# Kernel tuning notes

Hardware: AMD Instinct MI355X
Metric: run time of the kernel (lower is better)

## Reference

```python
import jax, jax.numpy as jnp
import numpy as np

RATIO = 1.0 / 32  # spacial_ratio
HOUT = 7          # pooled_h
WOUT = 7          # pooled_w
S = 2             # sub_bin_size = int(sqrt(n_sampled=4))


def setup_inputs() -> dict:
    key = jax.random.key(0)
    k1, k2, k3, k4, k5, k6 = jax.random.split(key, 6)
    B, C, H, W = 4, 256, 50, 50
    N = 1024
    img_w, img_h = W / RATIO, H / RATIO
    features = jax.random.normal(k1, (B, C, H, W), dtype=jnp.float32)
    b = jax.random.randint(k2, (N,), 0, B).astype(jnp.float32)
    x1 = jax.random.uniform(k3, (N,), minval=0.0, maxval=img_w - 232.0)
    y1 = jax.random.uniform(k4, (N,), minval=0.0, maxval=img_h - 232.0)
    bw = jax.random.uniform(k5, (N,), minval=32.0, maxval=232.0)
    bh = jax.random.uniform(k6, (N,), minval=32.0, maxval=232.0)
    rois = jnp.stack([b, x1, y1, x1 + bw, y1 + bh], axis=1)  # [N, 5]
    return {"features": features, "rois": rois}


def _roi_align(features, rois):
    B, C, H, W = features.shape
    fW = jnp.float32(W)
    fH = jnp.float32(H)
    b_idx = rois[:, 0].astype(jnp.int32)            # [N]
    box = rois[:, 1:] * RATIO                       # [N, 4] in feature coords
    bx1 = jnp.clip(box[:, 0], 0.0, fW)
    by1 = jnp.clip(box[:, 1], 0.0, fH)
    bx2 = jnp.clip(box[:, 2], 0.0, fW)
    by2 = jnp.clip(box[:, 3], 0.0, fH)
    roi_valid = (bx2 - bx1 > 0) & (by2 - by1 > 0)   # [N]
    bin_w = (bx2 - bx1) / WOUT                      # [N]
    bin_h = (by2 - by1) / HOUT

    jj = jnp.arange(WOUT, dtype=jnp.float32)
    ii = jnp.arange(HOUT, dtype=jnp.float32)
    # bin edges; y2/x2 computed from the UNclamped start, then clamped (matches original order)
    x1u = bx1[:, None] + jj * bin_w[:, None]        # [N, WOUT]
    x2b = jnp.clip(x1u + bin_w[:, None], 0.0, fW)
    x1b = jnp.clip(x1u, 0.0, fW)
    y1u = by1[:, None] + ii * bin_h[:, None]        # [N, HOUT]
    y2b = jnp.clip(y1u + bin_h[:, None], 0.0, fH)
    y1b = jnp.clip(y1u, 0.0, fH)
    bin_valid = (y2b > y1b)[:, :, None] & (x2b > x1b)[:, None, :]  # [N, HOUT, WOUT]

    # SxS sample-point centers inside each bin (sub_bin = bin / S, center offset 0.5)
    cc = jnp.arange(S, dtype=jnp.float32) + 0.5
    px = x1b[:, :, None] + cc * (bin_w / S)[:, None, None]  # [N, WOUT, S]
    py = y1b[:, :, None] + cc * (bin_h / S)[:, None, None]  # [N, HOUT, S]

    xl = jnp.clip(jnp.floor(px), 0, W - 1).astype(jnp.int32)
    xh = jnp.clip(xl + 1, 0, W - 1)
    yl = jnp.clip(jnp.floor(py), 0, H - 1).astype(jnp.int32)
    yh = jnp.clip(yl + 1, 0, H - 1)
    wxh = px - xl  # (x - x1)
    wxl = xh - px  # (x2 - x)
    wyb = py - yl  # (y - y1)
    wyt = yh - py  # (y2 - y)

    feats = features.transpose(0, 2, 3, 1)          # [B, H, W, C]
    bI = b_idx[:, None, None, None, None]           # [N,1,1,1,1]
    # x varies over (WOUT, sx) -> broadcast axes (2,4); y over (HOUT, sy) -> axes (1,3)
    XL = xl[:, None, :, None, :]
    XH = xh[:, None, :, None, :]
    YL = yl[:, :, None, :, None]
    YH = yh[:, :, None, :, None]
    WXh = wxh[:, None, :, None, :, None]
    WXl = wxl[:, None, :, None, :, None]
    WYb = wyb[:, :, None, :, None, None]
    WYt = wyt[:, :, None, :, None, None]

    v_tl = feats[bI, YL, XL]   # [N, HOUT, WOUT, S, S, C]
    v_tr = feats[bI, YL, XH]
    v_bl = feats[bI, YH, XL]
    v_br = feats[bI, YH, XH]
    top = WXh * v_tr + WXl * v_tl
    bot = WXh * v_br + WXl * v_bl
    val = WYb * bot + WYt * top                     # [N, HOUT, WOUT, S, S, C]

    pooled = val.max(axis=(3, 4))                   # max over sample grid -> [N, HOUT, WOUT, C]
    mask = bin_valid & roi_valid[:, None, None]
    pooled = jnp.where(mask[..., None], pooled, 0.0)
    return pooled.transpose(0, 3, 1, 2)             # [N, C, HOUT, WOUT]


def reference(features, rois):
    return _roi_align(features, rois)
```

## Files before the change

kernel.cpp:

```cpp
#include <hip/hip_runtime.h>


namespace {

constexpr int B_ = 4, C_ = 256, H_ = 50, W_ = 50;
constexpr int HW = H_ * W_;
constexpr int HO = 7, WO = 7, NBIN = HO * WO;
constexpr int OUT_PER_ROI = C_ * NBIN;
constexpr int LD = 260;
constexpr float RATIO = 1.0f / 32.0f;

__global__ __launch_bounds__(256) void transpose_tiled(
    const float* __restrict__ f, float* __restrict__ ft)
{
    __shared__ float tile[64][65];
    const int bt   = blockIdx.x;
    const int hw_t = bt % 40;
    const int c_t  = (bt / 40) % 4;
    const int b    = bt / 160;
    const int hw0 = hw_t * 64, c0 = c_t * 64;
    const int lx = threadIdx.x & 63;
    const int ly = threadIdx.x >> 6;

#pragma unroll
    for (int k = 0; k < 16; ++k) {
        const int c  = c0 + k * 4 + ly;
        const int hw = hw0 + lx;
        if (hw < HW)
            tile[k * 4 + ly][lx] = f[((size_t)b * C_ + c) * HW + hw];
    }
    __syncthreads();
#pragma unroll
    for (int k = 0; k < 16; ++k) {
        const int hw = hw0 + k * 4 + ly;
        if (hw < HW)
            ft[((size_t)b * HW + hw) * C_ + c0 + lx] = tile[lx][k * 4 + ly];
    }
}

template<int AX, int AY>
__device__ __forceinline__ float4 bin_max(const float4 p[3][3],
                                          const float4 wa, const float4 wb)
{
    float4 s[2][2];
#pragma unroll
    for (int sy = 0; sy < 2; ++sy) {
#pragma unroll
        for (int sx = 0; sx < 2; ++sx) {
            const int xk = AX * sx, yj = AY * sy;
            const float wxh = sx ? wa.y : wa.x;
            const float wxl = sx ? wa.w : wa.z;
            const float wyb = sy ? wb.y : wb.x;
            const float wyt = sy ? wb.w : wb.z;
            const float4 tl = p[yj][xk],     tr = p[yj][xk + 1];
            const float4 bl = p[yj + 1][xk], br = p[yj + 1][xk + 1];
            float4 o;
            o.x = wyb * (wxh * br.x + wxl * bl.x) + wyt * (wxh * tr.x + wxl * tl.x);
            o.y = wyb * (wxh * br.y + wxl * bl.y) + wyt * (wxh * tr.y + wxl * tl.y);
            o.z = wyb * (wxh * br.z + wxl * bl.z) + wyt * (wxh * tr.z + wxl * tl.z);
            o.w = wyb * (wxh * br.w + wxl * bl.w) + wyt * (wxh * tr.w + wxl * tl.w);
            s[sy][sx] = o;
        }
    }
    float4 m;
    m.x = fmaxf(fmaxf(s[0][0].x, s[0][1].x), fmaxf(s[1][0].x, s[1][1].x));
    m.y = fmaxf(fmaxf(s[0][0].y, s[0][1].y), fmaxf(s[1][0].y, s[1][1].y));
    m.z = fmaxf(fmaxf(s[0][0].z, s[0][1].z), fmaxf(s[1][0].z, s[1][1].z));
    m.w = fmaxf(fmaxf(s[0][0].w, s[0][1].w), fmaxf(s[1][0].w, s[1][1].w));
    return m;
}

__global__ __launch_bounds__(256) void roialign_main(
    const float* __restrict__ ft,
    const float* __restrict__ rois,
    float* __restrict__ out)
{
    __shared__ float stage[NBIN * LD];
    __shared__ __align__(16) float    wts[NBIN][8];
    __shared__ __align__(16) unsigned offp[NBIN][12];

    const int n    = blockIdx.x;
    const int tid  = threadIdx.x;
    const int wave = tid >> 6;
    const int lane = tid & 63;
    const float fW = (float)W_, fH = (float)H_;

    if (tid < NBIN) {
        const int ii = tid / WO, jj = tid % WO;
        const float* r = rois + n * 5;
        const float bx1 = fminf(fmaxf(r[1] * RATIO, 0.0f), fW);
        const float by1 = fminf(fmaxf(r[2] * RATIO, 0.0f), fH);
        const float bx2 = fminf(fmaxf(r[3] * RATIO, 0.0f), fW);
        const float by2 = fminf(fmaxf(r[4] * RATIO, 0.0f), fH);
        const bool roi_valid = (bx2 - bx1 > 0.0f) && (by2 - by1 > 0.0f);
        const float bin_w = (bx2 - bx1) * (1.0f / (float)WO);
        const float bin_h = (by2 - by1) * (1.0f / (float)HO);

        const float x1u = bx1 + (float)jj * bin_w;
        const float x1b = fminf(fmaxf(x1u, 0.0f), fW);
        const float x2b = fminf(fmaxf(x1u + bin_w, 0.0f), fW);
        const float y1u = by1 + (float)ii * bin_h;
        const float y1b = fminf(fmaxf(y1u, 0.0f), fH);
        const float y2b = fminf(fmaxf(y1u + bin_h, 0.0f), fH);
        const float vf = (roi_valid && (y2b > y1b) && (x2b > x1b)) ? 1.0f : 0.0f;

        int xl[2], yl[2];
#pragma unroll
        for (int s = 0; s < 2; ++s) {
            const float px = x1b + ((float)s + 0.5f) * (bin_w * 0.5f);
            int l = (int)floorf(px);
            l = min(max(l, 0), W_ - 1);
            const int h = min(l + 1, W_ - 1);
            xl[s] = l;
            wts[tid][0 + s] = vf * (px - (float)l);
            wts[tid][2 + s] = vf * ((float)h - px);

            const float py = y1b + ((float)s + 0.5f) * (bin_h * 0.5f);
            int t = (int)floorf(py);
            t = min(max(t, 0), H_ - 1);
            const int u = min(t + 1, H_ - 1);
            yl[s] = t;
            wts[tid][4 + s] = py - (float)t;
            wts[tid][6 + s] = (float)u - py;
        }
        const int X0 = xl[0], Y0 = yl[0];
        const int ax = min(xl[1] - X0, 1);
        const int ay = min(yl[1] - Y0, 1);
        const int pxs0 = X0, pxs1 = min(X0 + 1, W_ - 1), pxs2 = min(X0 + 2, W_ - 1);
        const int pys0 = Y0, pys1 = min(Y0 + 1, H_ - 1), pys2 = min(Y0 + 2, H_ - 1);
        const int px_[3] = {pxs0, pxs1, pxs2};
        const int py_[3] = {pys0, pys1, pys2};
#pragma unroll
        for (int j = 0; j < 3; ++j)
#pragma unroll
            for (int k = 0; k < 3; ++k)
                offp[tid][j * 3 + k] = (unsigned)(py_[j] * W_ + px_[k]);
        offp[tid][9]  = (unsigned)(ax | (ay << 1));
        offp[tid][10] = 0u;
        offp[tid][11] = 0u;
    }
    __syncthreads();

    int b = (int)rois[n * 5];
    b = min(max(b, 0), B_ - 1);
    const float4* pb = (const float4*)(ft + (size_t)b * HW * C_) + lane;

    for (int bin = wave; bin < NBIN; bin += 4) {
        const float4 wa = *(const float4*)wts[bin];
        const float4 wb = *(const float4*)(wts[bin] + 4);
        const uint4 o0 = *(const uint4*)&offp[bin][0];
        const uint4 o1 = *(const uint4*)&offp[bin][4];
        const uint2 o2 = *(const uint2*)&offp[bin][8];

        float4 p[3][3];
        p[0][0] = pb[(int)o0.x << 6];
        p[0][1] = pb[(int)o0.y << 6];
        p[0][2] = pb[(int)o0.z << 6];
        p[1][0] = pb[(int)o0.w << 6];
        p[1][1] = pb[(int)o1.x << 6];
        p[1][2] = pb[(int)o1.y << 6];
        p[2][0] = pb[(int)o1.z << 6];
        p[2][1] = pb[(int)o1.w << 6];
        p[2][2] = pb[(int)o2.x << 6];

        float4 m;
        switch (o2.y) {
            case 0u:  m = bin_max<0, 0>(p, wa, wb); break;
            case 1u:  m = bin_max<1, 0>(p, wa, wb); break;
            case 2u:  m = bin_max<0, 1>(p, wa, wb); break;
            default:  m = bin_max<1, 1>(p, wa, wb); break;
        }

        *(float4*)&stage[bin * LD + 4 * lane] = m;
    }
    __syncthreads();

    float* outn = out + (size_t)n * OUT_PER_ROI;
    for (int k = tid; k < OUT_PER_ROI; k += 256) {
        const int ch  = k / NBIN;
        const int bin = k - ch * NBIN;
        outn[k] = stage[bin * LD + ch];
    }
}

}

extern "C" void kernel_launch(void* const* d_in, const int* in_sizes, int n_in,
                              void* d_out, int out_size, void* d_ws, size_t ws_size,
                              hipStream_t stream)
{
    const float* feats = (const float*)d_in[0];
    const float* rois  = (const float*)d_in[1];
    float* out = (float*)d_out;
    const int N = in_sizes[1] / 5;
    float* ft = (float*)d_ws;

    hipLaunchKernelGGL(transpose_tiled, dim3(B_ * 4 * 40), dim3(256), 0, stream,
                       feats, ft);
    hipLaunchKernelGGL(roialign_main, dim3(N), dim3(256), 0, stream,
                       ft, rois, out);
}
```

Before: 101.8 us.

## Split each ROI across two blocks by channel half with float2 gathers

Each ROI is now handled by two blocks, each covering 128 channels, so the grid doubles and per-block shared staging shrinks to about half, allowing more resident blocks (launch bounds hint 5). Gathers go from float4 to float2 per lane, and bins are assigned to waves in contiguous balanced ranges instead of strided. Stage row stride changes to 129 to reduce bank conflicts on the transposed read. The per-bin setup (weights and offsets) is now computed twice per ROI, and narrower loads may lower memory efficiency.

```diff
diff --git a/kernel.cpp b/kernel.cpp
--- a/kernel.cpp
+++ b/kernel.cpp
@@ -6,8 +6,10 @@
 constexpr int B_ = 4, C_ = 256, H_ = 50, W_ = 50;
 constexpr int HW = H_ * W_;
 constexpr int HO = 7, WO = 7, NBIN = HO * WO;
+constexpr int CH = 128;
 constexpr int OUT_PER_ROI = C_ * NBIN;
-constexpr int LD = 260;
+constexpr int OUT_HALF = CH * NBIN;
+constexpr int LD = 129;
 constexpr float RATIO = 1.0f / 32.0f;
 
 __global__ __launch_bounds__(256) void transpose_tiled(
@@ -39,10 +41,10 @@
 }
 
 template<int AX, int AY>
-__device__ __forceinline__ float4 bin_max(const float4 p[3][3],
-                                          const float4 wa, const float4 wb)
-{
-    float4 s[2][2];
+__device__ __forceinline__ float2 bin_max2(const float2 p[3][3],
+                                           const float4 wa, const float4 wb)
+{
+    float2 s[2][2];
 #pragma unroll
     for (int sy = 0; sy < 2; ++sy) {
 #pragma unroll
@@ -52,25 +54,21 @@
             const float wxl = sx ? wa.w : wa.z;
             const float wyb = sy ? wb.y : wb.x;
             const float wyt = sy ? wb.w : wb.z;
-            const float4 tl = p[yj][xk],     tr = p[yj][xk + 1];
-            const float4 bl = p[yj + 1][xk], br = p[yj + 1][xk + 1];
-            float4 o;
+            const float2 tl = p[yj][xk],     tr = p[yj][xk + 1];
+            const float2 bl = p[yj + 1][xk], br = p[yj + 1][xk + 1];
+            float2 o;
             o.x = wyb * (wxh * br.x + wxl * bl.x) + wyt * (wxh * tr.x + wxl * tl.x);
             o.y = wyb * (wxh * br.y + wxl * bl.y) + wyt * (wxh * tr.y + wxl * tl.y);
-            o.z = wyb * (wxh * br.z + wxl * bl.z) + wyt * (wxh * tr.z + wxl * tl.z);
-            o.w = wyb * (wxh * br.w + wxl * bl.w) + wyt * (wxh * tr.w + wxl * tl.w);
             s[sy][sx] = o;
         }
     }
-    float4 m;
+    float2 m;
     m.x = fmaxf(fmaxf(s[0][0].x, s[0][1].x), fmaxf(s[1][0].x, s[1][1].x));
     m.y = fmaxf(fmaxf(s[0][0].y, s[0][1].y), fmaxf(s[1][0].y, s[1][1].y));
-    m.z = fmaxf(fmaxf(s[0][0].z, s[0][1].z), fmaxf(s[1][0].z, s[1][1].z));
-    m.w = fmaxf(fmaxf(s[0][0].w, s[0][1].w), fmaxf(s[1][0].w, s[1][1].w));
     return m;
 }
 
-__global__ __launch_bounds__(256) void roialign_main(
+__global__ __launch_bounds__(256, 5) void roialign_main(
     const float* __restrict__ ft,
     const float* __restrict__ rois,
     float* __restrict__ out)
@@ -79,7 +77,9 @@
     __shared__ __align__(16) float    wts[NBIN][8];
     __shared__ __align__(16) unsigned offp[NBIN][12];
 
-    const int n    = blockIdx.x;
+    const int bid  = blockIdx.x;
+    const int n    = bid >> 1;
+    const int half = bid & 1;
     const int tid  = threadIdx.x;
     const int wave = tid >> 6;
     const int lane = tid & 63;
@@ -143,40 +143,43 @@
 
     int b = (int)rois[n * 5];
     b = min(max(b, 0), B_ - 1);
-    const float4* pb = (const float4*)(ft + (size_t)b * HW * C_) + lane;
-
-    for (int bin = wave; bin < NBIN; bin += 4) {
+    const float2* pb = (const float2*)(ft + (size_t)b * HW * C_ + half * CH) + lane;
+
+    const int s0 = (wave * NBIN) >> 2;
+    const int e0 = ((wave + 1) * NBIN) >> 2;
+    for (int bin = s0; bin < e0; ++bin) {
         const float4 wa = *(const float4*)wts[bin];
         const float4 wb = *(const float4*)(wts[bin] + 4);
         const uint4 o0 = *(const uint4*)&offp[bin][0];
         const uint4 o1 = *(const uint4*)&offp[bin][4];
         const uint2 o2 = *(const uint2*)&offp[bin][8];
 
-        float4 p[3][3];
-        p[0][0] = pb[(int)o0.x << 6];
-        p[0][1] = pb[(int)o0.y << 6];
-        p[0][2] = pb[(int)o0.z << 6];
-        p[1][0] = pb[(int)o0.w << 6];
-        p[1][1] = pb[(int)o1.x << 6];
-        p[1][2] = pb[(int)o1.y << 6];
-        p[2][0] = pb[(int)o1.z << 6];
-        p[2][1] = pb[(int)o1.w << 6];
-        p[2][2] = pb[(int)o2.x << 6];
-
-        float4 m;
+        float2 p[3][3];
+        p[0][0] = pb[(int)o0.x << 7];
+        p[0][1] = pb[(int)o0.y << 7];
+        p[0][2] = pb[(int)o0.z << 7];
+        p[1][0] = pb[(int)o0.w << 7];
+        p[1][1] = pb[(int)o1.x << 7];
+        p[1][2] = pb[(int)o1.y << 7];
+        p[2][0] = pb[(int)o1.z << 7];
+        p[2][1] = pb[(int)o1.w << 7];
+        p[2][2] = pb[(int)o2.x << 7];
+
+        float2 m;
         switch (o2.y) {
-            case 0u:  m = bin_max<0, 0>(p, wa, wb); break;
-            case 1u:  m = bin_max<1, 0>(p, wa, wb); break;
-            case 2u:  m = bin_max<0, 1>(p, wa, wb); break;
-            default:  m = bin_max<1, 1>(p, wa, wb); break;
+            case 0u:  m = bin_max2<0, 0>(p, wa, wb); break;
+            case 1u:  m = bin_max2<1, 0>(p, wa, wb); break;
+            case 2u:  m = bin_max2<0, 1>(p, wa, wb); break;
+            default:  m = bin_max2<1, 1>(p, wa, wb); break;
         }
 
-        *(float4*)&stage[bin * LD + 4 * lane] = m;
+        stage[bin * LD + 2 * lane]     = m.x;
+        stage[bin * LD + 2 * lane + 1] = m.y;
     }
     __syncthreads();
 
-    float* outn = out + (size_t)n * OUT_PER_ROI;
-    for (int k = tid; k < OUT_PER_ROI; k += 256) {
+    float* outn = out + (size_t)n * OUT_PER_ROI + (size_t)half * OUT_HALF;
+    for (int k = tid; k < OUT_HALF; k += 256) {
         const int ch  = k / NBIN;
         const int bin = k - ch * NBIN;
         outn[k] = stage[bin * LD + ch];
@@ -197,6 +200,6 @@
 
     hipLaunchKernelGGL(transpose_tiled, dim3(B_ * 4 * 40), dim3(256), 0, stream,
                        feats, ft);
-    hipLaunchKernelGGL(roialign_main, dim3(N), dim3(256), 0, stream,
+    hipLaunchKernelGGL(roialign_main, dim3(N * 2), dim3(256), 0, stream,
                        ft, rois, out);
 }
```

Result: slower. 107.9 us (+6.0%).
